# Kernel optimization log

Measured on AMD Instinct MI355X. Metric: run time of the kernel, lower is better.

## Reference

```python
import jax, jax.numpy as jnp
import numpy as np

N_NODES = 4096
N_EDGES = 16384
F_IN = 64
F_EDGE = 16
HID = 128
OUT = 64
N_GRAPHS = 32


def _encoder(x, edge_index, edge_attr, batch, p):
    N = x.shape[0]
    src, dst = edge_index[0], edge_index[1]
    # EdgeMLP: [E, F_edge] -> [E, F_in * HID] per-edge weight matrices
    h = jax.nn.relu(edge_attr @ p['e_w1'] + p['e_b1'])
    h = jax.nn.relu(h @ p['e_w2'] + p['e_b2'])
    Wmat = (h @ p['e_w3'] + p['e_b3']).reshape(-1, x.shape[1], p['root_w'].shape[1])  # [E, F_in, HID]
    # NNConv: message = x_src @ W_edge, scatter-add to dst, plus root transform + bias
    msg = jnp.einsum('ei,eio->eo', x[src], Wmat)  # [E, HID]
    agg = jax.ops.segment_sum(msg, dst, num_segments=N)
    h1 = jax.nn.relu(agg + x @ p['root_w'] + p['conv1_b'])  # [N, HID]
    # GATConv (1 head, concat=False) with self-loops (PyG default)
    loop = jnp.arange(N, dtype=src.dtype)
    si = jnp.concatenate([src, loop])
    di = jnp.concatenate([dst, loop])
    hp = h1 @ p['gat_w']  # [N, HID]
    a_s = hp @ p['att_src']  # [N]
    a_d = hp @ p['att_dst']  # [N]
    e = jax.nn.leaky_relu(a_s[si] + a_d[di], negative_slope=0.2)
    m = jax.ops.segment_max(e, di, num_segments=N)
    ex = jnp.exp(e - m[di])
    denom = jax.ops.segment_sum(ex, di, num_segments=N)
    alpha = ex / (denom[di] + 1e-16)
    h2 = jax.ops.segment_sum(alpha[:, None] * hp[si], di, num_segments=N) + p['gat_b']
    h2 = jax.nn.relu(h2)
    # global mean pool over graphs
    s = jax.ops.segment_sum(h2, batch, num_segments=N_GRAPHS)
    cnt = jax.ops.segment_sum(jnp.ones((N,), h2.dtype), batch, num_segments=N_GRAPHS)
    pooled = s / jnp.maximum(cnt, 1.0)[:, None]
    return jax.nn.relu(pooled @ p['fc1_w'] + p['fc1_b'])  # [B, OUT]


def setup_inputs() -> dict:
    key = jax.random.key(0)
    ks = jax.random.split(key, 24)
    d = {}
    d['x1'] = jax.random.normal(ks[0], (N_NODES, F_IN), jnp.float32)
    d['edge_index1'] = jax.random.randint(ks[1], (2, N_EDGES), 0, N_NODES)
    d['edge_attr1'] = jax.random.normal(ks[2], (N_EDGES, F_EDGE), jnp.float32)
    d['batch1'] = jnp.sort(jax.random.randint(ks[3], (N_NODES,), 0, N_GRAPHS))
    d['x2'] = jax.random.normal(ks[4], (N_NODES, F_IN), jnp.float32)
    d['edge_index2'] = jax.random.randint(ks[5], (2, N_EDGES), 0, N_NODES)
    d['edge_attr2'] = jax.random.normal(ks[6], (N_EDGES, F_EDGE), jnp.float32)
    d['batch2'] = jnp.sort(jax.random.randint(ks[7], (N_NODES,), 0, N_GRAPHS))

    def lin(k, fi, fo):
        return jax.random.normal(k, (fi, fo), jnp.float32) * (fi ** -0.5)

    d['e_w1'] = lin(ks[8], F_EDGE, 128); d['e_b1'] = jnp.zeros((128,), jnp.float32)
    d['e_w2'] = lin(ks[9], 128, 64); d['e_b2'] = jnp.zeros((64,), jnp.float32)
    d['e_w3'] = lin(ks[10], 64, F_IN * HID); d['e_b3'] = jnp.zeros((F_IN * HID,), jnp.float32)
    d['root_w'] = lin(ks[11], F_IN, HID); d['conv1_b'] = jnp.zeros((HID,), jnp.float32)
    d['gat_w'] = lin(ks[12], HID, HID)
    d['att_src'] = jax.random.normal(ks[13], (HID,), jnp.float32) * (HID ** -0.5)
    d['att_dst'] = jax.random.normal(ks[14], (HID,), jnp.float32) * (HID ** -0.5)
    d['gat_b'] = jnp.zeros((HID,), jnp.float32)
    d['fc1_w'] = lin(ks[15], HID, OUT); d['fc1_b'] = jnp.zeros((OUT,), jnp.float32)
    d['fc2_w'] = lin(ks[16], OUT, 1); d['fc2_b'] = jnp.zeros((1,), jnp.float32)
    return d


def reference(x1, edge_index1, edge_attr1, batch1, x2, edge_index2, edge_attr2, batch2,
              e_w1, e_b1, e_w2, e_b2, e_w3, e_b3, root_w, conv1_b,
              gat_w, att_src, att_dst, gat_b, fc1_w, fc1_b, fc2_w, fc2_b):
    p = dict(e_w1=e_w1, e_b1=e_b1, e_w2=e_w2, e_b2=e_b2, e_w3=e_w3, e_b3=e_b3,
             root_w=root_w, conv1_b=conv1_b, gat_w=gat_w, att_src=att_src,
             att_dst=att_dst, gat_b=gat_b, fc1_w=fc1_w, fc1_b=fc1_b,
             fc2_w=fc2_w, fc2_b=fc2_b)
    z1 = _encoder(x1, edge_index1, edge_attr1, batch1, p)
    z2 = _encoder(x2, edge_index2, edge_attr2, batch2, p)
    z = jnp.abs(z1 - z2) @ fc2_w + fc2_b  # [B, 1]
    return jax.nn.sigmoid(z).squeeze(1)  # [B]
```

## Files before the change

kernel.cpp:

```cpp
#include <hip/hip_runtime.h>
#include <hip/hip_bf16.h>
#include <math.h>

#define NN 4096
#define NE 16384
#define FIN 64
#define FE 16
#define HIDD 128
#define OUTD 64
#define NG 32
#define EP (NE + NN)
#define KSPLIT 2
#define NCH (64 / KSPLIT)

typedef __attribute__((ext_vector_type(4))) unsigned u4v;
typedef __attribute__((ext_vector_type(4))) float f4v;
typedef _Float16 f16x8 __attribute__((ext_vector_type(8)));
typedef __fp16 fp16x2 __attribute__((ext_vector_type(2)));

union FragH { u4v u; f16x8 h; };
union H2U { fp16x2 v; unsigned u; };

__global__ void k_splitB(const float* __restrict__ w3, unsigned short* __restrict__ B1t) {
    __shared__ float lds[64 * 129];
    int c = blockIdx.x, t = threadIdx.x;
#pragma unroll
    for (int r = 0; r < 32; ++r) {
        int idx = r * 256 + t;
        lds[(idx >> 7) * 129 + (idx & 127)] = w3[(size_t)c * 8192 + idx];
    }
    __syncthreads();
#pragma unroll
    for (int r = 0; r < 32; ++r) {
        int e = r * 256 + t;
        float v = lds[(e & 63) * 129 + (e >> 6)];
        union { _Float16 f; unsigned short u; } cv;
        cv.f = (_Float16)v;
        B1t[(size_t)c * 8192 + e] = cv.u;
    }
}

#define PB_EMLP  4096
#define PB_BIAS  (PB_EMLP + 4096)
#define PB_TOTAL (PB_BIAS + 32)

__global__ void k_prep(const float* __restrict__ ea0, const float* __restrict__ ea1,
                       const float* __restrict__ w1, const float* __restrict__ b1,
                       const float* __restrict__ w2, const float* __restrict__ b2,
                       const float* __restrict__ X0, const float* __restrict__ X1,
                       const float* __restrict__ b3,
                       const int* __restrict__ ei0, const int* __restrict__ ei1,
                       float* __restrict__ h0, float* __restrict__ h1g,
                       float* __restrict__ Bb0, float* __restrict__ Bb1,
                       int* __restrict__ rowcnt) {
    int b = blockIdx.x, t = threadIdx.x;
    if (b < PB_EMLP) {
        int gi = b >> 11;
        int e0 = (b & 2047) * 8;
        const float* ea = gi ? ea1 : ea0;
        float* hout = gi ? h1g : h0;
        __shared__ float h1s[8][HIDD];
#pragma unroll
        for (int r = 0; r < 4; ++r) {
            int idx = r * 256 + t;
            int e1 = idx >> 7, j = idx & 127;
            float acc = b1[j];
#pragma unroll
            for (int i = 0; i < FE; ++i) acc += ea[(e0 + e1) * FE + i] * w1[i * HIDD + j];
            h1s[e1][j] = fmaxf(acc, 0.f);
        }
        __syncthreads();
#pragma unroll
        for (int r = 0; r < 2; ++r) {
            int idx = r * 256 + t;
            int e1 = idx >> 6, j = idx & 63;
            float acc = b2[j];
#pragma unroll 16
            for (int k = 0; k < HIDD; ++k) acc += h1s[e1][k] * w2[k * 64 + j];
            hout[(size_t)(e0 + e1) * 64 + j] = fmaxf(acc, 0.f);
        }
    } else if (b < PB_BIAS) {
        int bb = b - PB_EMLP;
        int gi = bb >> 11;
        int n = (bb & 2047) * 2 + (t >> 7);
        int o = t & 127;
        const float* X = gi ? X1 : X0;
        float* Bb = gi ? Bb1 : Bb0;
        float acc = 0.f;
#pragma unroll 16
        for (int i = 0; i < FIN; ++i) acc += X[n * FIN + i] * b3[i * HIDD + o];
        Bb[(size_t)n * HIDD + o] = acc;
    } else {
        int tid = (b - PB_BIAS) * 256 + t;
        for (int idx = tid; idx < 2 * EP; idx += 32 * 256) {
            int gi = idx / EP, e = idx % EP;
            const int* dst = (gi ? ei1 : ei0) + NE;
            int d = (e < NE) ? dst[e] : e - NE;
            atomicAdd(&rowcnt[gi * NN + d], 1);
        }
    }
}

__global__ void k_scan(const int* __restrict__ rowcnt, int* __restrict__ rowptr,
                       const int* __restrict__ batch0, const int* __restrict__ batch1,
                       int* __restrict__ br) {
    int b = blockIdx.x;
    if (b < 2) {
        int gi = b;
        const int* cnt = rowcnt + gi * NN;
        int* rp = rowptr + gi * (NN + 1);
        int t = threadIdx.x;
        int base = t * 4;
        int v0 = cnt[base], v1 = cnt[base + 1], v2 = cnt[base + 2], v3 = cnt[base + 3];
        int s = v0 + v1 + v2 + v3;
        __shared__ int sc[1024];
        sc[t] = s;
        __syncthreads();
        for (int off = 1; off < 1024; off <<= 1) {
            int a = (t >= off) ? sc[t - off] : 0;
            __syncthreads();
            sc[t] += a;
            __syncthreads();
        }
        int run = sc[t] - s;
        rp[base] = run; run += v0;
        rp[base + 1] = run; run += v1;
        rp[base + 2] = run; run += v2;
        rp[base + 3] = run; run += v3;
        if (t == 1023) rp[NN] = run;
    } else {
        int t = threadIdx.x;
        if (t < 66) {
            int gi = t / 33, g = t % 33;
            const int* batch = gi ? batch1 : batch0;
            int lo = 0, hi = NN;
            while (lo < hi) {
                int mid = (lo + hi) >> 1;
                if (batch[mid] < g) lo = mid + 1; else hi = mid;
            }
            br[gi * 33 + g] = lo;
        }
    }
}

__global__ void k_fill(const int* __restrict__ ei0, const int* __restrict__ ei1,
                       const int* __restrict__ rowptr, int* __restrict__ cnt2,
                       int* __restrict__ adj) {
    int idx = blockIdx.x * 256 + threadIdx.x;
    if (idx >= 2 * EP) return;
    int gi = idx / EP, e = idx % EP;
    const int* dst = (gi ? ei1 : ei0) + NE;
    int d = (e < NE) ? dst[e] : e - NE;
    int pos = rowptr[gi * (NN + 1) + d] + atomicAdd(&cnt2[gi * NN + d], 1);
    adj[gi * EP + pos] = e;
}

__global__ void __launch_bounds__(128, 2)
k_nnconv(const float* __restrict__ x0, const float* __restrict__ x1,
         const float* __restrict__ h_0, const float* __restrict__ h_1,
         const unsigned short* __restrict__ B1t,
         const float* __restrict__ Bb0, const float* __restrict__ Bb1,
         const int* __restrict__ ei0, const int* __restrict__ ei1,
         float* __restrict__ msg) {
    __shared__ __align__(16) float sm[64 * 128];
    int gi = blockIdx.z;
    const float* x = gi ? x1 : x0;
    const float* hh = gi ? h_1 : h_0;
    const float* Bb = gi ? Bb1 : Bb0;
    const int* src = gi ? ei1 : ei0;

    int t = threadIdx.x;
    int e0 = blockIdx.x * 64;
    int z = blockIdx.y;
    int ch = t >> 6;
    int l = t & 63, q4 = l >> 4, c16 = l & 15;

    FragH xhi[4][2], xlo[4][2];
#pragma unroll
    for (int mf = 0; mf < 4; ++mf) {
        int s_ = src[e0 + mf * 16 + c16];
        const float* xr = &x[(size_t)s_ * FIN];
#pragma unroll
        for (int kf = 0; kf < 2; ++kf) {
            float xv[8];
            *(float4*)&xv[0] = *(const float4*)&xr[kf * 32 + q4 * 8];
            *(float4*)&xv[4] = *(const float4*)&xr[kf * 32 + q4 * 8 + 4];
            u4v whi, wlo;
#pragma unroll
            for (int p = 0; p < 4; ++p) {
                H2U hi2, lo2;
                hi2.v = __builtin_amdgcn_cvt_pkrtz(xv[2 * p], xv[2 * p + 1]);
                float r0 = xv[2 * p] - (float)hi2.v[0];
                float r1 = xv[2 * p + 1] - (float)hi2.v[1];
                lo2.v = __builtin_amdgcn_cvt_pkrtz(r0, r1);
                whi[p] = hi2.u; wlo[p] = lo2.u;
            }
            xhi[mf][kf].u = whi; xlo[mf][kf].u = wlo;
        }
    }

    f4v acc[4][4];
#pragma unroll
    for (int a = 0; a < 4; ++a)
#pragma unroll
        for (int b = 0; b < 4; ++b) acc[a][b] = (f4v){0.f, 0.f, 0.f, 0.f};

    const u4v* bp = (const u4v*)B1t;

#define LOADF(buf, cg)                                                          \
    {                                                                           \
        const u4v* cp = bp + (size_t)(cg) * 1024;                               \
        _Pragma("unroll") for (int kf = 0; kf < 2; ++kf)                        \
        _Pragma("unroll") for (int nf = 0; nf < 4; ++nf)                        \
            buf[kf * 4 + nf].u = cp[(ch * 64 + nf * 16 + c16) * 8 + kf * 4 + q4]; \
    }

#define DOMFMA(buf, COMP)                                                       \
    {                                                                           \
        _Pragma("unroll") for (int mf = 0; mf < 4; ++mf) {                      \
            float hvf = hv4[mf].COMP;                                           \
            H2U hp2; hp2.v = __builtin_amdgcn_cvt_pkrtz(hvf, hvf);              \
            unsigned hw = hp2.u;                                                \
            FragH hb; hb.u = (u4v){hw, hw, hw, hw};                             \
            _Pragma("unroll") for (int kf = 0; kf < 2; ++kf) {                  \
                FragH a1, a2;                                                   \
                a1.h = hb.h * xhi[mf][kf].h;                                    \
                a2.h = hb.h * xlo[mf][kf].h;                                    \
                _Pragma("unroll") for (int nf = 0; nf < 4; ++nf) {              \
                    acc[mf][nf] = __builtin_amdgcn_mfma_f32_16x16x32_f16(       \
                        a1.h, buf[kf * 4 + nf].h, acc[mf][nf], 0, 0, 0);        \
                    acc[mf][nf] = __builtin_amdgcn_mfma_f32_16x16x32_f16(       \
                        a2.h, buf[kf * 4 + nf].h, acc[mf][nf], 0, 0, 0);        \
                }                                                               \
            }                                                                   \
        }                                                                       \
    }

    FragH bA[8], bB[8];
    float4 hv4[4];
    LOADF(bA, z * NCH);
#pragma unroll 1
    for (int cl = 0; cl < NCH; cl += 4) {
#pragma unroll
        for (int mf = 0; mf < 4; ++mf)
            hv4[mf] = *(const float4*)&hh[(size_t)(e0 + mf * 16 + c16) * 64 + z * NCH + cl];
        LOADF(bB, z * NCH + cl + 1);
        DOMFMA(bA, x);
        LOADF(bA, z * NCH + cl + 2);
        DOMFMA(bB, y);
        LOADF(bB, z * NCH + cl + 3);
        DOMFMA(bA, z);
        if (cl + 4 < NCH) LOADF(bA, z * NCH + cl + 4);
        DOMFMA(bB, w);
    }
#undef LOADF
#undef DOMFMA

    float* mb = msg + (size_t)(gi * KSPLIT + z) * NE * HIDD;
#pragma unroll
    for (int mf = 0; mf < 4; ++mf)
#pragma unroll
        for (int j = 0; j < 4; ++j) {
            int rr = mf * 16 + q4 * 4 + j;
#pragma unroll
            for (int nf = 0; nf < 4; ++nf)
                sm[rr * 128 + ch * 64 + nf * 16 + c16] = acc[mf][nf][j];
        }
    __syncthreads();
    int z0 = (z == 0);
#pragma unroll
    for (int it = 0; it < 16; ++it) {
        int f = it * 128 + t;
        int row = f >> 5, c4 = f & 31;
        int eg = e0 + row;
        float4 v = *(float4*)&sm[row * 128 + c4 * 4];
        if (z0) {
            int s_ = src[eg];
            const float* bbr = &Bb[(size_t)s_ * HIDD + c4 * 4];
            v.x += bbr[0]; v.y += bbr[1]; v.z += bbr[2]; v.w += bbr[3];
        }
        *(float4*)&mb[(size_t)eg * HIDD + c4 * 4] = v;
    }
}

__global__ void k_h1hp(const float* __restrict__ msg,
                       const int* __restrict__ rowptr, const int* __restrict__ adj,
                       const float* __restrict__ X0, const float* __restrict__ X1,
                       const float* __restrict__ rw, const float* __restrict__ cb,
                       const float* __restrict__ gw,
                       const float* __restrict__ asw, const float* __restrict__ adw,
                       float* __restrict__ hp0, float* __restrict__ hp1,
                       float* __restrict__ a_s0, float* __restrict__ a_s1,
                       float* __restrict__ a_d0, float* __restrict__ a_d1) {
    int gi = blockIdx.y;
    const float* X = gi ? X1 : X0;
    float* hp = gi ? hp1 : hp0;
    float* a_s = gi ? a_s1 : a_s0;
    float* a_d = gi ? a_d1 : a_d0;
    const int* rp = rowptr + gi * (NN + 1);
    const int* aj = adj + gi * EP;
    const float* mz0 = msg + (size_t)(gi * KSPLIT + 0) * NE * HIDD;
    const float* mz1 = msg + (size_t)(gi * KSPLIT + 1) * NE * HIDD;
    int n0 = blockIdx.x * 4;
    int o = threadIdx.x;
    __shared__ float xsh[4][FIN];
    __shared__ float h1s[4][HIDD];
    __shared__ float s1[4][2], s2[4][2];
    xsh[o >> 6][o & 63] = X[n0 * FIN + o];
    xsh[2 + (o >> 6)][o & 63] = X[n0 * FIN + 128 + o];
    __syncthreads();
    float accs[4];
#pragma unroll
    for (int nn = 0; nn < 4; ++nn) {
        int n = n0 + nn;
        float acc = cb[o];
        int lo = rp[n], hi = rp[n + 1];
        for (int p = lo; p < hi; ++p) {
            int e = aj[p];
            if (e < NE) acc += mz0[(size_t)e * HIDD + o] + mz1[(size_t)e * HIDD + o];
        }
        accs[nn] = acc;
    }
#pragma unroll 8
    for (int i = 0; i < FIN; ++i) {
        float w = rw[i * HIDD + o];
#pragma unroll
        for (int nn = 0; nn < 4; ++nn) accs[nn] += xsh[nn][i] * w;
    }
#pragma unroll
    for (int nn = 0; nn < 4; ++nn) h1s[nn][o] = fmaxf(accs[nn], 0.f);
    __syncthreads();
#pragma unroll
    for (int nn = 0; nn < 4; ++nn) accs[nn] = 0.f;
#pragma unroll 8
    for (int k = 0; k < HIDD; ++k) {
        float w = gw[k * HIDD + o];
#pragma unroll
        for (int nn = 0; nn < 4; ++nn) accs[nn] += h1s[nn][k] * w;
    }
#pragma unroll
    for (int nn = 0; nn < 4; ++nn) {
        hp[(size_t)(n0 + nn) * HIDD + o] = accs[nn];
        float p1 = accs[nn] * asw[o], p2 = accs[nn] * adw[o];
#pragma unroll
        for (int off = 32; off; off >>= 1) {
            p1 += __shfl_down(p1, off);
            p2 += __shfl_down(p2, off);
        }
        if ((o & 63) == 0) { s1[nn][o >> 6] = p1; s2[nn][o >> 6] = p2; }
    }
    __syncthreads();
    if (o < 4) {
        a_s[n0 + o] = s1[o][0] + s1[o][1];
        a_d[n0 + o] = s2[o][0] + s2[o][1];
    }
}

__global__ void k_gat(const int* __restrict__ rowptr, const int* __restrict__ adj,
                      const int* __restrict__ ei0, const int* __restrict__ ei1,
                      const float* __restrict__ hp0, const float* __restrict__ hp1,
                      const float* __restrict__ as0, const float* __restrict__ as1,
                      const float* __restrict__ ad0, const float* __restrict__ ad1,
                      const float* __restrict__ gb,
                      float* __restrict__ h2_0, float* __restrict__ h2_1) {
    int gi = blockIdx.y;
    const int* src = gi ? ei1 : ei0;
    const float* hp = gi ? hp1 : hp0;
    const float* a_s = gi ? as1 : as0;
    const float* a_d = gi ? ad1 : ad0;
    float* h2 = gi ? h2_1 : h2_0;
    const int* rp = rowptr + gi * (NN + 1);
    const int* aj = adj + gi * EP;
    int w = threadIdx.x >> 6, l = threadIdx.x & 63;
    int n = blockIdx.x * 4 + w;
    int lo = rp[n], deg = rp[n + 1] - lo;
    float adn = a_d[n];
    float m = -1e30f;
    for (int base = 0; base < deg; base += 64) {
        float sc = -1e30f;
        int j = base + l;
        if (j < deg) {
            int e = aj[lo + j];
            int si = (e < NE) ? src[e] : n;
            float xsc = a_s[si] + adn;
            sc = xsc > 0.f ? xsc : 0.2f * xsc;
        }
#pragma unroll
        for (int off = 32; off; off >>= 1) sc = fmaxf(sc, __shfl_xor(sc, off));
        m = fmaxf(m, sc);
    }
    float den = 0.f;
    for (int base = 0; base < deg; base += 64) {
        float ev = 0.f;
        int j = base + l;
        if (j < deg) {
            int e = aj[lo + j];
            int si = (e < NE) ? src[e] : n;
            float xsc = a_s[si] + adn;
            float sc = xsc > 0.f ? xsc : 0.2f * xsc;
            ev = expf(sc - m);
        }
#pragma unroll
        for (int off = 32; off; off >>= 1) ev += __shfl_xor(ev, off);
        den += ev;
    }
    float inv = 1.f / (den + 1e-16f);
    float acc0 = 0.f, acc1 = 0.f;
    for (int j = 0; j < deg; ++j) {
        int e = aj[lo + j];
        int si = (e < NE) ? src[e] : n;
        float xsc = a_s[si] + adn;
        float sc = xsc > 0.f ? xsc : 0.2f * xsc;
        float al = expf(sc - m) * inv;
        acc0 += al * hp[(size_t)si * HIDD + l];
        acc1 += al * hp[(size_t)si * HIDD + 64 + l];
    }
    h2[(size_t)n * HIDD + l] = fmaxf(acc0 + gb[l], 0.f);
    h2[(size_t)n * HIDD + 64 + l] = fmaxf(acc1 + gb[64 + l], 0.f);
}

__global__ void k_poolfc1(const float* __restrict__ h2_0, const float* __restrict__ h2_1,
                          const int* __restrict__ br,
                          const float* __restrict__ w, const float* __restrict__ bias,
                          float* __restrict__ z) {
    int gi = blockIdx.x >> 5, g = blockIdx.x & 31;
    const float* h2 = gi ? h2_1 : h2_0;
    int lo = br[gi * 33 + g], hi = br[gi * 33 + g + 1];
    int t = threadIdx.x;
    __shared__ float pool[HIDD];
    float acc = 0.f;
    for (int n = lo; n < hi; ++n) acc += h2[(size_t)n * HIDD + t];
    pool[t] = acc;
    __syncthreads();
    if (t < 64) {
        float c = fmaxf((float)(hi - lo), 1.f);
        float a = bias[t];
#pragma unroll 16
        for (int o = 0; o < HIDD; ++o) a += (pool[o] / c) * w[o * OUTD + t];
        z[gi * NG * OUTD + g * OUTD + t] = fmaxf(a, 0.f);
    }
}

__global__ void k_final(const float* __restrict__ zz,
                        const float* __restrict__ w, const float* __restrict__ b,
                        float* __restrict__ out) {
    int g = threadIdx.x;
    const float* z1 = zz;
    const float* z2 = zz + NG * OUTD;
    float acc = b[0];
#pragma unroll
    for (int j = 0; j < OUTD; ++j) acc += fabsf(z1[g * OUTD + j] - z2[g * OUTD + j]) * w[j];
    out[g] = 1.f / (1.f + expf(-acc));
}

extern "C" void kernel_launch(void* const* d_in, const int* in_sizes, int n_in,
                              void* d_out, int out_size, void* d_ws, size_t ws_size,
                              hipStream_t stream) {
    const float* x0     = (const float*)d_in[0];
    const int*   ei0    = (const int*)d_in[1];
    const float* ea0    = (const float*)d_in[2];
    const int*   b0     = (const int*)d_in[3];
    const float* x1     = (const float*)d_in[4];
    const int*   ei1    = (const int*)d_in[5];
    const float* ea1    = (const float*)d_in[6];
    const int*   b1     = (const int*)d_in[7];
    const float* e_w1 = (const float*)d_in[8];
    const float* e_b1 = (const float*)d_in[9];
    const float* e_w2 = (const float*)d_in[10];
    const float* e_b2 = (const float*)d_in[11];
    const float* e_w3 = (const float*)d_in[12];
    const float* e_b3 = (const float*)d_in[13];
    const float* root_w = (const float*)d_in[14];
    const float* conv1_b = (const float*)d_in[15];
    const float* gat_w = (const float*)d_in[16];
    const float* att_src = (const float*)d_in[17];
    const float* att_dst = (const float*)d_in[18];
    const float* gat_b = (const float*)d_in[19];
    const float* fc1_w = (const float*)d_in[20];
    const float* fc1_b = (const float*)d_in[21];
    const float* fc2_w = (const float*)d_in[22];
    const float* fc2_b = (const float*)d_in[23];

    float* ws = (float*)d_ws;
    size_t off = 0;
    auto alloc = [&](size_t n) { float* p = ws + off; off += n; return p; };
    int* rowcnt = (int*)alloc(2 * NN);
    int* cnt2   = (int*)alloc(2 * NN);
    size_t zero_elems = off;
    int* rowptr = (int*)alloc(2 * (NN + 1));
    int* br     = (int*)alloc(66);
    int* adj    = (int*)alloc(2 * EP);
    float* h[2]   = {alloc((size_t)NE * 64), alloc((size_t)NE * 64)};
    unsigned short* B1t = (unsigned short*)alloc((size_t)4096 * 128 / 2);
    float* Bb[2]  = {alloc((size_t)NN * HIDD), alloc((size_t)NN * HIDD)};
    float* msg    = alloc((size_t)2 * KSPLIT * NE * HIDD);
    float* hp[2]  = {alloc((size_t)NN * HIDD), alloc((size_t)NN * HIDD)};
    float* a_s[2] = {alloc(NN), alloc(NN)};
    float* a_d[2] = {alloc(NN), alloc(NN)};
    float* h2[2]  = {alloc((size_t)NN * HIDD), alloc((size_t)NN * HIDD)};
    float* zz     = alloc((size_t)2 * NG * OUTD);

    (void)hipMemsetAsync(ws, 0, zero_elems * 4, stream);
    k_splitB<<<64, 256, 0, stream>>>(e_w3, B1t);
    k_prep<<<PB_TOTAL, 256, 0, stream>>>(ea0, ea1, e_w1, e_b1, e_w2, e_b2,
                                         x0, x1, e_b3, ei0, ei1,
                                         h[0], h[1], Bb[0], Bb[1],
                                         rowcnt);
    k_scan<<<3, 1024, 0, stream>>>(rowcnt, rowptr, b0, b1, br);
    k_fill<<<(2 * EP + 255) / 256, 256, 0, stream>>>(ei0, ei1, rowptr, cnt2, adj);
    k_nnconv<<<dim3(NE / 64, KSPLIT, 2), 128, 0, stream>>>(
        x0, x1, h[0], h[1], B1t, Bb[0], Bb[1], ei0, ei1, msg);
    k_h1hp<<<dim3(NN / 4, 2), HIDD, 0, stream>>>(
        msg, rowptr, adj, x0, x1, root_w, conv1_b, gat_w, att_src, att_dst,
        hp[0], hp[1], a_s[0], a_s[1], a_d[0], a_d[1]);
    k_gat<<<dim3(NN / 4, 2), 256, 0, stream>>>(
        rowptr, adj, ei0, ei1, hp[0], hp[1], a_s[0], a_s[1], a_d[0], a_d[1],
        gat_b, h2[0], h2[1]);
    k_poolfc1<<<64, HIDD, 0, stream>>>(h2[0], h2[1], br, fc1_w, fc1_b, zz);
    k_final<<<1, NG, 0, stream>>>(zz, fc2_w, fc2_b, (float*)d_out);
}
```

Measured before the change: 243.7 us.

## Drop fp16 hi/lo split in NNConv MFMA and raise K-split to four

The x operand is now converted to a single fp16 value instead of a hi+lo pair, which halves the MFMA count in the NNConv inner loop. KSPLIT rises from 2 to 4 with launch bounds of 4 blocks per SM, and the LDS staging buffer is halved by writing results out in two 32-row passes. The aggregation kernel now sums four partial message buffers. This trades accuracy (losing the residual correction term), extra msg write and read traffic, and an extra sync for fewer MFMAs and higher occupancy.

```diff
diff --git a/kernel.cpp b/kernel.cpp
--- a/kernel.cpp
+++ b/kernel.cpp
@@ -10,16 +10,15 @@
 #define OUTD 64
 #define NG 32
 #define EP (NE + NN)
-#define KSPLIT 2
+#define KSPLIT 4
 #define NCH (64 / KSPLIT)
 
 typedef __attribute__((ext_vector_type(4))) unsigned u4v;
 typedef __attribute__((ext_vector_type(4))) float f4v;
 typedef _Float16 f16x8 __attribute__((ext_vector_type(8)));
-typedef __fp16 fp16x2 __attribute__((ext_vector_type(2)));
 
 union FragH { u4v u; f16x8 h; };
-union H2U { fp16x2 v; unsigned u; };
+union FH2 { _Float16 f[2]; unsigned u; };
 
 __global__ void k_splitB(const float* __restrict__ w3, unsigned short* __restrict__ B1t) {
     __shared__ float lds[64 * 129];
@@ -155,14 +154,14 @@
     adj[gi * EP + pos] = e;
 }
 
-__global__ void __launch_bounds__(128, 2)
+__global__ void __launch_bounds__(128, 4)
 k_nnconv(const float* __restrict__ x0, const float* __restrict__ x1,
          const float* __restrict__ h_0, const float* __restrict__ h_1,
          const unsigned short* __restrict__ B1t,
          const float* __restrict__ Bb0, const float* __restrict__ Bb1,
          const int* __restrict__ ei0, const int* __restrict__ ei1,
          float* __restrict__ msg) {
-    __shared__ __align__(16) float sm[64 * 128];
+    __shared__ __align__(16) float sm[32 * 128];
     int gi = blockIdx.z;
     const float* x = gi ? x1 : x0;
     const float* hh = gi ? h_1 : h_0;
@@ -175,7 +174,7 @@
     int ch = t >> 6;
     int l = t & 63, q4 = l >> 4, c16 = l & 15;
 
-    FragH xhi[4][2], xlo[4][2];
+    FragH xf[4][2];
 #pragma unroll
     for (int mf = 0; mf < 4; ++mf) {
         int s_ = src[e0 + mf * 16 + c16];
@@ -185,17 +184,15 @@
             float xv[8];
             *(float4*)&xv[0] = *(const float4*)&xr[kf * 32 + q4 * 8];
             *(float4*)&xv[4] = *(const float4*)&xr[kf * 32 + q4 * 8 + 4];
-            u4v whi, wlo;
+            u4v w;
 #pragma unroll
             for (int p = 0; p < 4; ++p) {
-                H2U hi2, lo2;
-                hi2.v = __builtin_amdgcn_cvt_pkrtz(xv[2 * p], xv[2 * p + 1]);
-                float r0 = xv[2 * p] - (float)hi2.v[0];
-                float r1 = xv[2 * p + 1] - (float)hi2.v[1];
-                lo2.v = __builtin_amdgcn_cvt_pkrtz(r0, r1);
-                whi[p] = hi2.u; wlo[p] = lo2.u;
+                FH2 c2;
+                c2.f[0] = (_Float16)xv[2 * p];
+                c2.f[1] = (_Float16)xv[2 * p + 1];
+                w[p] = c2.u;
             }
-            xhi[mf][kf].u = whi; xlo[mf][kf].u = wlo;
+            xf[mf][kf].u = w;
         }
     }
 
@@ -218,19 +215,17 @@
 #define DOMFMA(buf, COMP)                                                       \
     {                                                                           \
         _Pragma("unroll") for (int mf = 0; mf < 4; ++mf) {                      \
-            float hvf = hv4[mf].COMP;                                           \
-            H2U hp2; hp2.v = __builtin_amdgcn_cvt_pkrtz(hvf, hvf);              \
+            FH2 hp2;                                                            \
+            hp2.f[0] = (_Float16)hv4[mf].COMP;                                  \
+            hp2.f[1] = hp2.f[0];                                                \
             unsigned hw = hp2.u;                                                \
             FragH hb; hb.u = (u4v){hw, hw, hw, hw};                             \
             _Pragma("unroll") for (int kf = 0; kf < 2; ++kf) {                  \
-                FragH a1, a2;                                                   \
-                a1.h = hb.h * xhi[mf][kf].h;                                    \
-                a2.h = hb.h * xlo[mf][kf].h;                                    \
+                FragH a1;                                                       \
+                a1.h = hb.h * xf[mf][kf].h;                                     \
                 _Pragma("unroll") for (int nf = 0; nf < 4; ++nf) {              \
                     acc[mf][nf] = __builtin_amdgcn_mfma_f32_16x16x32_f16(       \
                         a1.h, buf[kf * 4 + nf].h, acc[mf][nf], 0, 0, 0);        \
-                    acc[mf][nf] = __builtin_amdgcn_mfma_f32_16x16x32_f16(       \
-                        a2.h, buf[kf * 4 + nf].h, acc[mf][nf], 0, 0, 0);        \
                 }                                                               \
             }                                                                   \
         }                                                                       \
@@ -257,29 +252,35 @@
 #undef DOMFMA
 
     float* mb = msg + (size_t)(gi * KSPLIT + z) * NE * HIDD;
-#pragma unroll
-    for (int mf = 0; mf < 4; ++mf)
-#pragma unroll
-        for (int j = 0; j < 4; ++j) {
-            int rr = mf * 16 + q4 * 4 + j;
-#pragma unroll
-            for (int nf = 0; nf < 4; ++nf)
-                sm[rr * 128 + ch * 64 + nf * 16 + c16] = acc[mf][nf][j];
-        }
-    __syncthreads();
     int z0 = (z == 0);
 #pragma unroll
-    for (int it = 0; it < 16; ++it) {
-        int f = it * 128 + t;
-        int row = f >> 5, c4 = f & 31;
-        int eg = e0 + row;
-        float4 v = *(float4*)&sm[row * 128 + c4 * 4];
-        if (z0) {
-            int s_ = src[eg];
-            const float* bbr = &Bb[(size_t)s_ * HIDD + c4 * 4];
-            v.x += bbr[0]; v.y += bbr[1]; v.z += bbr[2]; v.w += bbr[3];
-        }
-        *(float4*)&mb[(size_t)eg * HIDD + c4 * 4] = v;
+    for (int half = 0; half < 2; ++half) {
+        if (half) __syncthreads();
+#pragma unroll
+        for (int mf2 = 0; mf2 < 2; ++mf2) {
+            int mf = half * 2 + mf2;
+#pragma unroll
+            for (int j = 0; j < 4; ++j) {
+                int rr = mf2 * 16 + q4 * 4 + j;
+#pragma unroll
+                for (int nf = 0; nf < 4; ++nf)
+                    sm[rr * 128 + ch * 64 + nf * 16 + c16] = acc[mf][nf][j];
+            }
+        }
+        __syncthreads();
+#pragma unroll
+        for (int it = 0; it < 8; ++it) {
+            int f = it * 128 + t;
+            int row = f >> 5, c4 = f & 31;
+            int eg = e0 + half * 32 + row;
+            float4 v = *(float4*)&sm[row * 128 + c4 * 4];
+            if (z0) {
+                int s_ = src[eg];
+                const float* bbr = &Bb[(size_t)s_ * HIDD + c4 * 4];
+                v.x += bbr[0]; v.y += bbr[1]; v.z += bbr[2]; v.w += bbr[3];
+            }
+            *(float4*)&mb[(size_t)eg * HIDD + c4 * 4] = v;
+        }
     }
 }
 
@@ -301,6 +302,8 @@
     const int* aj = adj + gi * EP;
     const float* mz0 = msg + (size_t)(gi * KSPLIT + 0) * NE * HIDD;
     const float* mz1 = msg + (size_t)(gi * KSPLIT + 1) * NE * HIDD;
+    const float* mz2 = msg + (size_t)(gi * KSPLIT + 2) * NE * HIDD;
+    const float* mz3 = msg + (size_t)(gi * KSPLIT + 3) * NE * HIDD;
     int n0 = blockIdx.x * 4;
     int o = threadIdx.x;
     __shared__ float xsh[4][FIN];
@@ -317,7 +320,10 @@
         int lo = rp[n], hi = rp[n + 1];
         for (int p = lo; p < hi; ++p) {
             int e = aj[p];
-            if (e < NE) acc += mz0[(size_t)e * HIDD + o] + mz1[(size_t)e * HIDD + o];
+            if (e < NE) {
+                size_t eo = (size_t)e * HIDD + o;
+                acc += (mz0[eo] + mz1[eo]) + (mz2[eo] + mz3[eo]);
+            }
         }
         accs[nn] = acc;
     }
```

Result: slower. 613.3 us (+151.7%).
